# Kernel optimization log

Hardware: AMD Instinct MI355X
Metric: run time of the kernel (lower is better)

The kernel has to match this reference:

```python
import jax, jax.numpy as jnp
import numpy as np

N = 20000
N_RET = 20000
NEG_SLOPE = 0.2


def _xavier(key, shape):
    fan_in, fan_out = shape[-2], shape[-1]
    limit = float(np.sqrt(6.0 / (fan_in + fan_out)))
    return jax.random.uniform(key, shape, jnp.float32, -limit, limit)


def setup_inputs() -> dict:
    key = jax.random.key(0)
    ks = jax.random.split(key, 24)
    E = 320000
    inp = {
        "emb_u": jax.random.normal(ks[0], (N, 256), jnp.float32),
        "emb_t": jax.random.normal(ks[1], (N, 256), jnp.float32),
        "src_u": jax.random.randint(ks[2], (E,), 0, N, jnp.int32),
        "trg_u": jax.random.randint(ks[3], (E,), 0, N, jnp.int32),
        "src_t": jax.random.randint(ks[4], (E,), 0, N, jnp.int32),
        "trg_t": jax.random.randint(ks[5], (E,), 0, N, jnp.int32),
    }
    # SpGATLayer params per stack (u=user graph, t=tweet graph), 2 layers each.
    # layer0: f_in=256, layer1: f_in = 64*4 = 256 (concat of heads); f_out=64, H=4.
    i = 6
    for side in ("u", "t"):
        for l in range(2):
            inp[f"w_{side}{l}"] = _xavier(ks[i], (4, 256, 64)); i += 1
            inp[f"a_src_{side}{l}"] = _xavier(ks[i], (4, 64, 1))[:, :, 0]; i += 1
            inp[f"a_trg_{side}{l}"] = _xavier(ks[i], (4, 64, 1))[:, :, 0]; i += 1
    inp["fc_w"] = _xavier(ks[i], (128, 16)); i += 1  # [in_features, out_features]
    inp["fc_b"] = jnp.zeros((16,), jnp.float32)
    return inp


def gat_layer(h, w, a_src, a_trg, src, trg):
    # h: [n, f_in], w: [H, f_in, F], a_*: [H, F]
    hp = jnp.einsum("nf,hfo->hno", h, w)                 # [H, n, F]
    attn_src = jnp.einsum("hno,ho->nh", hp, a_src)        # [n, H]
    attn_trg = jnp.einsum("hno,ho->nh", hp, a_trg)        # [n, H]
    e = jax.nn.leaky_relu(attn_src[src] + attn_trg[trg], NEG_SLOPE)  # [E, H]
    exp_e = jnp.exp(e - jnp.max(e))
    denom = jax.ops.segment_sum(exp_e, trg, num_segments=N)[trg] + 1e-16
    attn = (exp_e / denom)[:, :, None]                    # [E, H, 1]
    hp_lift = jnp.transpose(hp, (1, 0, 2))[src]           # [E, H, F]
    return jax.ops.segment_sum(hp_lift * attn, trg, num_segments=N)  # [n, H, F]


def run_stack(h, src, trg, w0, as0, at0, w1, as1, at1):
    x = gat_layer(h, w0, as0, at0, src, trg)
    x = jax.nn.elu(x.reshape(N, -1))                      # [n, H*F]
    x = gat_layer(x, w1, as1, at1, src, trg)
    return x.mean(axis=1)                                 # [n, F]


def reference(emb_u, emb_t, src_u, trg_u, src_t, trg_t,
              w_u0, a_src_u0, a_trg_u0, w_u1, a_src_u1, a_trg_u1,
              w_t0, a_src_t0, a_trg_t0, w_t1, a_src_t1, a_trg_t1,
              fc_w, fc_b):
    out_u = run_stack(emb_u, src_u, trg_u, w_u0, a_src_u0, a_trg_u0, w_u1, a_src_u1, a_trg_u1)
    out_t = run_stack(emb_t, src_t, trg_t, w_t0, a_src_t0, a_trg_t0, w_t1, a_src_t1, a_trg_t1)
    ret = jnp.concatenate([out_u[:N_RET], out_t[:N_RET]], axis=-1)   # [n_ret, 128]
    logits = ret @ fc_w + fc_b                                       # [n_ret, 16]
    return jax.nn.log_softmax(logits, axis=-1)
```

## Files before the change

### kernel.cpp

```cpp
#include <hip/hip_runtime.h>
#include <hip/hip_bf16.h>

#define NEG_SLOPE 0.2f

typedef unsigned short u16;
typedef u16 u16x8 __attribute__((ext_vector_type(8)));
typedef u16 u16x4 __attribute__((ext_vector_type(4)));
typedef short s16x8 __attribute__((ext_vector_type(8)));
typedef float f32x4 __attribute__((ext_vector_type(4)));

__device__ __forceinline__ u16 f2bf(float x) {
    unsigned u = __float_as_uint(x);
    return (u16)((u + 0x7fffu + ((u >> 16) & 1u)) >> 16);
}
__device__ __forceinline__ float bf2f(u16 h) {
    return __uint_as_float(((unsigned)h) << 16);
}

__global__ __launch_bounds__(256) void splitx_k(
    const float* __restrict__ x0, const float* __restrict__ x1,
    u16* __restrict__ Xh, u16* __restrict__ Xl, int per_side4)
{
    int i = blockIdx.x * 256 + threadIdx.x;
    if (i >= per_side4) return;
    int side = blockIdx.y;
    const float* X = side ? x1 : x0;
    size_t o = (size_t)side * per_side4 * 4 + (size_t)i * 4;
    float4 v = *(const float4*)(X + (size_t)i * 4);
    float f[4] = { v.x, v.y, v.z, v.w };
    u16x4 hi, lo;
    #pragma unroll
    for (int j = 0; j < 4; ++j) {
        u16 h = f2bf(f[j]);
        hi[j] = h;
        lo[j] = f2bf(f[j] - bf2f(h));
    }
    *(u16x4*)(Xh + o) = hi;
    *(u16x4*)(Xl + o) = lo;
}

__global__ __launch_bounds__(256) void wsplit4_k(
    const float* __restrict__ w0, const float* __restrict__ w1,
    const float* __restrict__ w2, const float* __restrict__ w3,
    u16* __restrict__ Wht, u16* __restrict__ Wlt)
{
    int tid = blockIdx.x * 256 + threadIdx.x;
    int which = tid >> 16;
    int idx = tid & 65535;
    const float* W = (which == 0) ? w0 : (which == 1) ? w1 : (which == 2) ? w2 : w3;
    int f = idx & 63, k = (idx >> 6) & 255, h = idx >> 14;
    float x = W[idx];
    u16 hi = f2bf(x);
    u16 lo = f2bf(x - bf2f(hi));
    int o = (which << 16) + (h * 64 + f) * 256 + k;
    Wht[o] = hi; Wlt[o] = lo;
}

__global__ __launch_bounds__(256) void gemm_mfma_k(
    const u16* __restrict__ xh_all, const u16* __restrict__ xl_all,
    const u16* __restrict__ Wht, const u16* __restrict__ Wlt,
    const float* __restrict__ au_s, const float* __restrict__ au_t,
    const float* __restrict__ at_s, const float* __restrict__ at_t,
    u16* __restrict__ hpb_all,
    float* __restrict__ asat,
    int layer, int n)
{
    const int side = blockIdx.y;
    const int row0 = blockIdx.x * 64;
    const int t = threadIdx.x;
    const int l = t & 63;
    const int h = t >> 6;
    const int which = side * 2 + layer;

    const u16* Xh = xh_all + (size_t)side * n * 256;
    const u16* Xl = xl_all + (size_t)side * n * 256;
    const u16* Wh = Wht + ((size_t)which << 16);
    const u16* Wl = Wlt + ((size_t)which << 16);
    const float* a_src = (side ? at_s : au_s) + h * 64;
    const float* a_trg = (side ? at_t : au_t) + h * 64;
    u16* HPB = hpb_all + (size_t)side * n * 256;
    float* as_ = asat + (size_t)which * n * 8;
    float* at_ = as_ + (size_t)n * 4;

    __shared__ u16 Ah[64 * 40], Al[64 * 40], Bh[256 * 40], Bl[256 * 40];

    const int sr = t >> 2, sp = t & 3;
    const int arow = (row0 + sr < n) ? (row0 + sr) : (n - 1);
    const u16* gAh = Xh + (size_t)arow * 256 + sp * 8;
    const u16* gAl = Xl + (size_t)arow * 256 + sp * 8;
    const int lda = sr * 40 + sp * 8;

    const int fb = l & 15;
    const int kg = l >> 4;
    int ra[4], cb[4];
    #pragma unroll
    for (int r = 0; r < 4; ++r) ra[r] = (r * 16 + fb) * 40 + kg * 8;
    #pragma unroll
    for (int c = 0; c < 4; ++c) cb[c] = (h * 64 + c * 16 + fb) * 40 + kg * 8;

    f32x4 acc[4][4];
    #pragma unroll
    for (int r = 0; r < 4; ++r)
        #pragma unroll
        for (int c = 0; c < 4; ++c) acc[r][c] = f32x4{0.f, 0.f, 0.f, 0.f};

    for (int k0 = 0; k0 < 256; k0 += 32) {
        __syncthreads();
        *(u16x8*)&Ah[lda] = *(const u16x8*)(gAh + k0);
        *(u16x8*)&Al[lda] = *(const u16x8*)(gAl + k0);
        #pragma unroll
        for (int i = 0; i < 4; ++i) {
            int j = t + i * 256;
            int col = j >> 2, cp = j & 3;
            int ofs = col * 40 + cp * 8;
            *(u16x8*)&Bh[ofs] = *(const u16x8*)(Wh + (size_t)col * 256 + k0 + cp * 8);
            *(u16x8*)&Bl[ofs] = *(const u16x8*)(Wl + (size_t)col * 256 + k0 + cp * 8);
        }
        __syncthreads();

        s16x8 bh[4], bl[4];
        #pragma unroll
        for (int c = 0; c < 4; ++c) {
            bh[c] = *(const s16x8*)&Bh[cb[c]];
            bl[c] = *(const s16x8*)&Bl[cb[c]];
        }
        #pragma unroll
        for (int r = 0; r < 4; ++r) {
            s16x8 ah = *(const s16x8*)&Ah[ra[r]];
            s16x8 al = *(const s16x8*)&Al[ra[r]];
            #pragma unroll
            for (int c = 0; c < 4; ++c) {
                acc[r][c] = __builtin_amdgcn_mfma_f32_16x16x32_bf16(ah, bh[c], acc[r][c], 0, 0, 0);
                acc[r][c] = __builtin_amdgcn_mfma_f32_16x16x32_bf16(ah, bl[c], acc[r][c], 0, 0, 0);
                acc[r][c] = __builtin_amdgcn_mfma_f32_16x16x32_bf16(al, bh[c], acc[r][c], 0, 0, 0);
            }
        }
    }

    float pav[4], pbv[4];
    #pragma unroll
    for (int c = 0; c < 4; ++c) { pav[c] = a_src[c * 16 + fb]; pbv[c] = a_trg[c * 16 + fb]; }

    #pragma unroll
    for (int r = 0; r < 4; ++r) {
        #pragma unroll
        for (int q = 0; q < 4; ++q) {
            int grow = row0 + r * 16 + kg * 4 + q;
            float s = 0.f, u = 0.f;
            if (grow < n) {
                u16* hrow = HPB + (size_t)grow * 256 + h * 64 + fb;
                #pragma unroll
                for (int c = 0; c < 4; ++c) {
                    float v = acc[r][c][q];
                    s += v * pav[c];
                    u += v * pbv[c];
                    hrow[c * 16] = f2bf(v);
                }
            }
            #pragma unroll
            for (int off = 8; off; off >>= 1) {
                s += __shfl_xor(s, off, 16);
                u += __shfl_xor(u, off, 16);
            }
            if (grow < n && fb == 0) {
                as_[grow * 4 + h] = s;
                at_[grow * 4 + h] = u;
            }
        }
    }
}

__global__ void hist2_k(const int* __restrict__ tu, const int* __restrict__ tt,
                        int* __restrict__ counts, int* __restrict__ ranks,
                        int E, int N)
{
    int e = blockIdx.x * blockDim.x + threadIdx.x;
    if (e < E)          ranks[e] = atomicAdd(&counts[tu[e]], 1);
    else if (e < 2 * E) ranks[e] = atomicAdd(&counts[N + tt[e - E]], 1);
}

__global__ __launch_bounds__(1024) void scan2_k(const int* __restrict__ counts_all,
                                                int* __restrict__ starts_all, int n)
{
    const int T = 1024;
    const int* counts = counts_all + blockIdx.x * n;
    int* starts = starts_all + blockIdx.x * (n + 1);
    int t = threadIdx.x;
    int chunk = (n + T - 1) / T;
    int beg = t * chunk;
    int end = min(beg + chunk, n);
    int sum = 0;
    for (int i = beg; i < end; ++i) sum += counts[i];
    __shared__ int lds[T];
    lds[t] = sum;
    __syncthreads();
    for (int off = 1; off < T; off <<= 1) {
        int v = (t >= off) ? lds[t - off] : 0;
        __syncthreads();
        lds[t] += v;
        __syncthreads();
    }
    int run = lds[t] - sum;
    for (int i = beg; i < end; ++i) { starts[i] = run; run += counts[i]; }
    if (t == T - 1) starts[n] = lds[T - 1];
}

__global__ void scatter2_k(const int* __restrict__ su, const int* __restrict__ st,
                           const int* __restrict__ tu, const int* __restrict__ tt,
                           const int* __restrict__ starts_all,
                           const int* __restrict__ ranks, int* __restrict__ srcs,
                           int E, int N)
{
    int e = blockIdx.x * blockDim.x + threadIdx.x;
    if (e < E) {
        srcs[starts_all[tu[e]] + ranks[e]] = su[e];
    } else if (e < 2 * E) {
        int ee = e - E;
        const int* st1 = starts_all + (N + 1);
        srcs[E + st1[tt[ee]] + ranks[e]] = st[ee];
    }
}

template<int LAYER>
__global__ __launch_bounds__(256) void aggregate_k(
    const u16* __restrict__ hpb_all, const float* __restrict__ asat,
    const int* __restrict__ starts2, const int* __restrict__ srcs2,
    u16* __restrict__ oh_all, u16* __restrict__ ol_all,
    float* __restrict__ of_all, int n, int E)
{
    const int side = blockIdx.y;
    const int w = threadIdx.x >> 6;
    const int l = threadIdx.x & 63;
    const int v = blockIdx.x * 4 + w;
    if (v >= n) return;
    const int h = l >> 4;
    const int which = side * 2 + LAYER;

    const u16* HPB = hpb_all + (size_t)side * n * 256;
    const float* as_ = asat + (size_t)which * n * 8;
    const float* at_ = as_ + (size_t)n * 4;
    const int* starts = starts2 + side * (n + 1);
    const int* srcs = srcs2 + (size_t)side * E;

    const int s0 = starts[v], s1 = starts[v + 1];
    const float atv = at_[v * 4 + h];
    const size_t lo4 = (size_t)l * 4;

    float4 ac0 = make_float4(0.f, 0.f, 0.f, 0.f), ac1 = ac0, ac2 = ac0, ac3 = ac0;
    float dn0 = 0.f, dn1 = 0.f, dn2 = 0.f, dn3 = 0.f;

    for (int base = s0; base < s1; base += 64) {
        int m = min(64, s1 - base);
        int s_l = (base + l < s1) ? srcs[base + l] : 0;
        int i = 0;
        for (; i + 3 < m; i += 4) {
            int sa = __shfl(s_l, i, 64);
            int sb = __shfl(s_l, i + 1, 64);
            int sc = __shfl(s_l, i + 2, 64);
            int sd = __shfl(s_l, i + 3, 64);
            u16x4 va = *(const u16x4*)(HPB + (size_t)sa * 256 + lo4);
            u16x4 vb = *(const u16x4*)(HPB + (size_t)sb * 256 + lo4);
            u16x4 vc = *(const u16x4*)(HPB + (size_t)sc * 256 + lo4);
            u16x4 vd = *(const u16x4*)(HPB + (size_t)sd * 256 + lo4);
            float ea = as_[sa * 4 + h] + atv;
            float eb = as_[sb * 4 + h] + atv;
            float ec = as_[sc * 4 + h] + atv;
            float ed = as_[sd * 4 + h] + atv;
            ea = (ea > 0.f) ? ea : NEG_SLOPE * ea;
            eb = (eb > 0.f) ? eb : NEG_SLOPE * eb;
            ec = (ec > 0.f) ? ec : NEG_SLOPE * ec;
            ed = (ed > 0.f) ? ed : NEG_SLOPE * ed;
            float pA = expf(ea), pB = expf(eb), pC = expf(ec), pD = expf(ed);
            dn0 += pA; dn1 += pB; dn2 += pC; dn3 += pD;
            ac0.x += pA * bf2f(va[0]); ac0.y += pA * bf2f(va[1]);
            ac0.z += pA * bf2f(va[2]); ac0.w += pA * bf2f(va[3]);
            ac1.x += pB * bf2f(vb[0]); ac1.y += pB * bf2f(vb[1]);
            ac1.z += pB * bf2f(vb[2]); ac1.w += pB * bf2f(vb[3]);
            ac2.x += pC * bf2f(vc[0]); ac2.y += pC * bf2f(vc[1]);
            ac2.z += pC * bf2f(vc[2]); ac2.w += pC * bf2f(vc[3]);
            ac3.x += pD * bf2f(vd[0]); ac3.y += pD * bf2f(vd[1]);
            ac3.z += pD * bf2f(vd[2]); ac3.w += pD * bf2f(vd[3]);
        }
        for (; i < m; ++i) {
            int sa = __shfl(s_l, i, 64);
            u16x4 va = *(const u16x4*)(HPB + (size_t)sa * 256 + lo4);
            float ea = as_[sa * 4 + h] + atv;
            ea = (ea > 0.f) ? ea : NEG_SLOPE * ea;
            float pA = expf(ea);
            dn0 += pA;
            ac0.x += pA * bf2f(va[0]); ac0.y += pA * bf2f(va[1]);
            ac0.z += pA * bf2f(va[2]); ac0.w += pA * bf2f(va[3]);
        }
    }

    float4 acc = make_float4(ac0.x + ac1.x + ac2.x + ac3.x,
                             ac0.y + ac1.y + ac2.y + ac3.y,
                             ac0.z + ac1.z + ac2.z + ac3.z,
                             ac0.w + ac1.w + ac2.w + ac3.w);
    float r = 1.f / (dn0 + dn1 + dn2 + dn3 + 1e-16f);
    acc.x *= r; acc.y *= r; acc.z *= r; acc.w *= r;

    if (LAYER == 0) {
        u16* oh = oh_all + (size_t)side * n * 256;
        u16* ol = ol_all + (size_t)side * n * 256;
        float f[4] = { acc.x, acc.y, acc.z, acc.w };
        u16x4 hi, lo;
        #pragma unroll
        for (int c = 0; c < 4; ++c) {
            float e = (f[c] > 0.f) ? f[c] : expm1f(f[c]);
            u16 hh = f2bf(e);
            hi[c] = hh;
            lo[c] = f2bf(e - bf2f(hh));
        }
        *(u16x4*)(oh + (size_t)v * 256 + lo4) = hi;
        *(u16x4*)(ol + (size_t)v * 256 + lo4) = lo;
    } else {
        float* of = of_all + (size_t)side * n * 64;
        acc.x += __shfl_xor(acc.x, 16, 64); acc.y += __shfl_xor(acc.y, 16, 64);
        acc.z += __shfl_xor(acc.z, 16, 64); acc.w += __shfl_xor(acc.w, 16, 64);
        acc.x += __shfl_xor(acc.x, 32, 64); acc.y += __shfl_xor(acc.y, 32, 64);
        acc.z += __shfl_xor(acc.z, 32, 64); acc.w += __shfl_xor(acc.w, 32, 64);
        if (l < 16) {
            acc.x *= 0.25f; acc.y *= 0.25f; acc.z *= 0.25f; acc.w *= 0.25f;
            *(float4*)(of + (size_t)v * 64 + l * 4) = acc;
        }
    }
}

__global__ __launch_bounds__(256) void final_k(
    const float* __restrict__ out_u, const float* __restrict__ out_t,
    const float* __restrict__ fcw, const float* __restrict__ fcb,
    float* __restrict__ out, int nret)
{
    int gid = blockIdx.x * blockDim.x + threadIdx.x;
    int nn = gid >> 4;
    int j  = gid & 15;
    if (nn >= nret) return;
    const float* ru = out_u + (size_t)nn * 64;
    const float* rt = out_t + (size_t)nn * 64;
    float acc = fcb[j];
    #pragma unroll 8
    for (int k = 0; k < 64; ++k) acc += ru[k] * fcw[k * 16 + j];
    #pragma unroll 8
    for (int k = 0; k < 64; ++k) acc += rt[k] * fcw[(64 + k) * 16 + j];

    float m = acc;
    for (int off = 8; off; off >>= 1) m = fmaxf(m, __shfl_xor(m, off, 16));
    float ex = expf(acc - m);
    float s = ex;
    for (int off = 8; off; off >>= 1) s += __shfl_xor(s, off, 16);
    out[(size_t)nn * 16 + j] = acc - m - logf(s);
}

extern "C" void kernel_launch(void* const* d_in, const int* in_sizes, int n_in,
                              void* d_out, int out_size, void* d_ws, size_t ws_size,
                              hipStream_t stream)
{
    const int N = in_sizes[0] / 256;
    const int E = in_sizes[2];
    const int NRET = out_size / 16;

    const float* emb[2]  = { (const float*)d_in[0], (const float*)d_in[1] };
    const int*   srcI[2] = { (const int*)d_in[2], (const int*)d_in[4] };
    const int*   trgI[2] = { (const int*)d_in[3], (const int*)d_in[5] };
    const float* fcw = (const float*)d_in[18];
    const float* fcb = (const float*)d_in[19];

    char* p = (char*)d_ws;
    u16* hpb  = (u16*)p;    p += (size_t)2 * N * 256 * 2;
    u16* xh   = (u16*)p;    p += (size_t)2 * N * 256 * 2;
    u16* xl   = (u16*)p;    p += (size_t)2 * N * 256 * 2;
    u16* wht  = (u16*)p;    p += (size_t)4 * 65536 * 2;
    u16* wlt  = (u16*)p;    p += (size_t)4 * 65536 * 2;
    float* asat = (float*)p; p += (size_t)4 * N * 8 * 4;
    float* outs = (float*)p; p += (size_t)2 * N * 64 * 4;
    int* starts2 = (int*)p; p += (size_t)2 * (N + 1) * 4;
    int* counts2 = (int*)p; p += (size_t)2 * N * 4;
    int* ranks2  = (int*)p; p += (size_t)2 * E * 4;
    int* srcs2   = (int*)p; p += (size_t)2 * E * 4;

    const int E2B = (2 * E + 255) / 256;
    const dim3 gemm_grid((N + 63) / 64, 2);
    const dim3 split_grid((N * 64 + 255) / 256, 2);
    const dim3 agg_grid((N + 3) / 4, 2);

    hipMemsetAsync(counts2, 0, (size_t)2 * N * 4, stream);

    hist2_k<<<E2B, 256, 0, stream>>>(trgI[0], trgI[1], counts2, ranks2, E, N);
    scan2_k<<<2, 1024, 0, stream>>>(counts2, starts2, N);
    scatter2_k<<<E2B, 256, 0, stream>>>(srcI[0], srcI[1], trgI[0], trgI[1],
                                        starts2, ranks2, srcs2, E, N);

    wsplit4_k<<<1024, 256, 0, stream>>>(
        (const float*)d_in[6], (const float*)d_in[9],
        (const float*)d_in[12], (const float*)d_in[15], wht, wlt);

    splitx_k<<<split_grid, 256, 0, stream>>>(emb[0], emb[1], xh, xl, N * 64);

    for (int layer = 0; layer < 2; ++layer) {
        const float* au_s = (const float*)d_in[6 + 0 * 6 + layer * 3 + 1];
        const float* au_t = (const float*)d_in[6 + 0 * 6 + layer * 3 + 2];
        const float* at_s = (const float*)d_in[6 + 1 * 6 + layer * 3 + 1];
        const float* at_t = (const float*)d_in[6 + 1 * 6 + layer * 3 + 2];

        gemm_mfma_k<<<gemm_grid, 256, 0, stream>>>(
            xh, xl, wht, wlt, au_s, au_t, at_s, at_t, hpb, asat, layer, N);

        if (layer == 0)
            aggregate_k<0><<<agg_grid, 256, 0, stream>>>(
                hpb, asat, starts2, srcs2, xh, xl, nullptr, N, E);
        else
            aggregate_k<1><<<agg_grid, 256, 0, stream>>>(
                hpb, asat, starts2, srcs2, nullptr, nullptr, outs, N, E);
    }

    final_k<<<(NRET * 16 + 255) / 256, 256, 0, stream>>>(
        outs, outs + (size_t)N * 64, fcw, fcb, (float*)d_out, NRET);
}
```

Measured before the change: 384.4 us.

## Precompute per-edge attention exponentials in separate kernel before aggregation

Adds a pexp_k kernel that computes the leaky-relu and exp attention weight once per edge and head, storing them in a new edge-ordered p4 buffer. The scatter kernel now also writes target ids in CSR order so this kernel can run. The aggregate kernel then reads the precomputed weights and source indices directly instead of recomputing exp redundantly across 16 lanes per head, and it drops the shuffle-based index broadcast. In exchange there is an extra kernel launch per layer plus extra global traffic for p4 and trgs, and it switches from expf to __expf.

```diff
diff --git a/kernel.cpp b/kernel.cpp
--- a/kernel.cpp
+++ b/kernel.cpp
@@ -208,22 +208,50 @@
 __global__ void scatter2_k(const int* __restrict__ su, const int* __restrict__ st,
                            const int* __restrict__ tu, const int* __restrict__ tt,
                            const int* __restrict__ starts_all,
-                           const int* __restrict__ ranks, int* __restrict__ srcs,
+                           const int* __restrict__ ranks,
+                           int* __restrict__ srcs, int* __restrict__ trgs,
                            int E, int N)
 {
     int e = blockIdx.x * blockDim.x + threadIdx.x;
     if (e < E) {
-        srcs[starts_all[tu[e]] + ranks[e]] = su[e];
+        int pos = starts_all[tu[e]] + ranks[e];
+        srcs[pos] = su[e];
+        trgs[pos] = tu[e];
     } else if (e < 2 * E) {
         int ee = e - E;
         const int* st1 = starts_all + (N + 1);
-        srcs[E + st1[tt[ee]] + ranks[e]] = st[ee];
-    }
+        int pos = E + st1[tt[ee]] + ranks[e];
+        srcs[pos] = st[ee];
+        trgs[pos] = tt[ee];
+    }
+}
+
+__global__ __launch_bounds__(256) void pexp_k(
+    const int* __restrict__ srcs2, const int* __restrict__ trgs2,
+    const float* __restrict__ asat, float* __restrict__ p4,
+    int layer, int n, int E)
+{
+    int j = blockIdx.x * 256 + threadIdx.x;
+    if (j >= E) return;
+    int side = blockIdx.y;
+    const float* as_ = asat + (size_t)(side * 2 + layer) * n * 8;
+    const float* at_ = as_ + (size_t)n * 4;
+    int s = srcs2[(size_t)side * E + j];
+    int v = trgs2[(size_t)side * E + j];
+    float4 a = *(const float4*)(as_ + s * 4);
+    float4 b = *(const float4*)(at_ + v * 4);
+    float4 p;
+    float x;
+    x = a.x + b.x; p.x = __expf(fmaxf(x, NEG_SLOPE * x));
+    x = a.y + b.y; p.y = __expf(fmaxf(x, NEG_SLOPE * x));
+    x = a.z + b.z; p.z = __expf(fmaxf(x, NEG_SLOPE * x));
+    x = a.w + b.w; p.w = __expf(fmaxf(x, NEG_SLOPE * x));
+    *(float4*)(p4 + ((size_t)side * E + j) * 4) = p;
 }
 
 template<int LAYER>
 __global__ __launch_bounds__(256) void aggregate_k(
-    const u16* __restrict__ hpb_all, const float* __restrict__ asat,
+    const u16* __restrict__ hpb_all, const float* __restrict__ p4,
     const int* __restrict__ starts2, const int* __restrict__ srcs2,
     u16* __restrict__ oh_all, u16* __restrict__ ol_all,
     float* __restrict__ of_all, int n, int E)
@@ -234,63 +262,43 @@
     const int v = blockIdx.x * 4 + w;
     if (v >= n) return;
     const int h = l >> 4;
-    const int which = side * 2 + LAYER;
-
-    const u16* HPB = hpb_all + (size_t)side * n * 256;
-    const float* as_ = asat + (size_t)which * n * 8;
-    const float* at_ = as_ + (size_t)n * 4;
+
+    const u16* hp_l = hpb_all + (size_t)side * n * 256 + l * 4;
     const int* starts = starts2 + side * (n + 1);
     const int* srcs = srcs2 + (size_t)side * E;
+    const float* pp = p4 + (size_t)side * E * 4 + h;
 
     const int s0 = starts[v], s1 = starts[v + 1];
-    const float atv = at_[v * 4 + h];
-    const size_t lo4 = (size_t)l * 4;
 
     float4 ac0 = make_float4(0.f, 0.f, 0.f, 0.f), ac1 = ac0, ac2 = ac0, ac3 = ac0;
     float dn0 = 0.f, dn1 = 0.f, dn2 = 0.f, dn3 = 0.f;
 
-    for (int base = s0; base < s1; base += 64) {
-        int m = min(64, s1 - base);
-        int s_l = (base + l < s1) ? srcs[base + l] : 0;
-        int i = 0;
-        for (; i + 3 < m; i += 4) {
-            int sa = __shfl(s_l, i, 64);
-            int sb = __shfl(s_l, i + 1, 64);
-            int sc = __shfl(s_l, i + 2, 64);
-            int sd = __shfl(s_l, i + 3, 64);
-            u16x4 va = *(const u16x4*)(HPB + (size_t)sa * 256 + lo4);
-            u16x4 vb = *(const u16x4*)(HPB + (size_t)sb * 256 + lo4);
-            u16x4 vc = *(const u16x4*)(HPB + (size_t)sc * 256 + lo4);
-            u16x4 vd = *(const u16x4*)(HPB + (size_t)sd * 256 + lo4);
-            float ea = as_[sa * 4 + h] + atv;
-            float eb = as_[sb * 4 + h] + atv;
-            float ec = as_[sc * 4 + h] + atv;
-            float ed = as_[sd * 4 + h] + atv;
-            ea = (ea > 0.f) ? ea : NEG_SLOPE * ea;
-            eb = (eb > 0.f) ? eb : NEG_SLOPE * eb;
-            ec = (ec > 0.f) ? ec : NEG_SLOPE * ec;
-            ed = (ed > 0.f) ? ed : NEG_SLOPE * ed;
-            float pA = expf(ea), pB = expf(eb), pC = expf(ec), pD = expf(ed);
-            dn0 += pA; dn1 += pB; dn2 += pC; dn3 += pD;
-            ac0.x += pA * bf2f(va[0]); ac0.y += pA * bf2f(va[1]);
-            ac0.z += pA * bf2f(va[2]); ac0.w += pA * bf2f(va[3]);
-            ac1.x += pB * bf2f(vb[0]); ac1.y += pB * bf2f(vb[1]);
-            ac1.z += pB * bf2f(vb[2]); ac1.w += pB * bf2f(vb[3]);
-            ac2.x += pC * bf2f(vc[0]); ac2.y += pC * bf2f(vc[1]);
-            ac2.z += pC * bf2f(vc[2]); ac2.w += pC * bf2f(vc[3]);
-            ac3.x += pD * bf2f(vd[0]); ac3.y += pD * bf2f(vd[1]);
-            ac3.z += pD * bf2f(vd[2]); ac3.w += pD * bf2f(vd[3]);
-        }
-        for (; i < m; ++i) {
-            int sa = __shfl(s_l, i, 64);
-            u16x4 va = *(const u16x4*)(HPB + (size_t)sa * 256 + lo4);
-            float ea = as_[sa * 4 + h] + atv;
-            ea = (ea > 0.f) ? ea : NEG_SLOPE * ea;
-            float pA = expf(ea);
-            dn0 += pA;
-            ac0.x += pA * bf2f(va[0]); ac0.y += pA * bf2f(va[1]);
-            ac0.z += pA * bf2f(va[2]); ac0.w += pA * bf2f(va[3]);
-        }
+    int j = s0;
+    for (; j + 3 < s1; j += 4) {
+        int sa = srcs[j], sb = srcs[j + 1], sc = srcs[j + 2], sd = srcs[j + 3];
+        float pA = pp[(j + 0) * 4], pB = pp[(j + 1) * 4];
+        float pC = pp[(j + 2) * 4], pD = pp[(j + 3) * 4];
+        u16x4 va = *(const u16x4*)(hp_l + sa * 256);
+        u16x4 vb = *(const u16x4*)(hp_l + sb * 256);
+        u16x4 vc = *(const u16x4*)(hp_l + sc * 256);
+        u16x4 vd = *(const u16x4*)(hp_l + sd * 256);
+        dn0 += pA; dn1 += pB; dn2 += pC; dn3 += pD;
+        ac0.x += pA * bf2f(va[0]); ac0.y += pA * bf2f(va[1]);
+        ac0.z += pA * bf2f(va[2]); ac0.w += pA * bf2f(va[3]);
+        ac1.x += pB * bf2f(vb[0]); ac1.y += pB * bf2f(vb[1]);
+        ac1.z += pB * bf2f(vb[2]); ac1.w += pB * bf2f(vb[3]);
+        ac2.x += pC * bf2f(vc[0]); ac2.y += pC * bf2f(vc[1]);
+        ac2.z += pC * bf2f(vc[2]); ac2.w += pC * bf2f(vc[3]);
+        ac3.x += pD * bf2f(vd[0]); ac3.y += pD * bf2f(vd[1]);
+        ac3.z += pD * bf2f(vd[2]); ac3.w += pD * bf2f(vd[3]);
+    }
+    for (; j < s1; ++j) {
+        int sa = srcs[j];
+        float pA = pp[j * 4];
+        u16x4 va = *(const u16x4*)(hp_l + sa * 256);
+        dn0 += pA;
+        ac0.x += pA * bf2f(va[0]); ac0.y += pA * bf2f(va[1]);
+        ac0.z += pA * bf2f(va[2]); ac0.w += pA * bf2f(va[3]);
     }
 
     float4 acc = make_float4(ac0.x + ac1.x + ac2.x + ac3.x,
@@ -312,8 +320,8 @@
             hi[c] = hh;
             lo[c] = f2bf(e - bf2f(hh));
         }
-        *(u16x4*)(oh + (size_t)v * 256 + lo4) = hi;
-        *(u16x4*)(ol + (size_t)v * 256 + lo4) = lo;
+        *(u16x4*)(oh + (size_t)v * 256 + l * 4) = hi;
+        *(u16x4*)(ol + (size_t)v * 256 + l * 4) = lo;
     } else {
         float* of = of_all + (size_t)side * n * 64;
         acc.x += __shfl_xor(acc.x, 16, 64); acc.y += __shfl_xor(acc.y, 16, 64);
@@ -374,22 +382,25 @@
     u16* wlt  = (u16*)p;    p += (size_t)4 * 65536 * 2;
     float* asat = (float*)p; p += (size_t)4 * N * 8 * 4;
     float* outs = (float*)p; p += (size_t)2 * N * 64 * 4;
+    float* p4   = (float*)p; p += (size_t)2 * E * 4 * 4;
     int* starts2 = (int*)p; p += (size_t)2 * (N + 1) * 4;
     int* counts2 = (int*)p; p += (size_t)2 * N * 4;
     int* ranks2  = (int*)p; p += (size_t)2 * E * 4;
     int* srcs2   = (int*)p; p += (size_t)2 * E * 4;
+    int* trgs2   = (int*)p; p += (size_t)2 * E * 4;
 
     const int E2B = (2 * E + 255) / 256;
     const dim3 gemm_grid((N + 63) / 64, 2);
     const dim3 split_grid((N * 64 + 255) / 256, 2);
     const dim3 agg_grid((N + 3) / 4, 2);
+    const dim3 pexp_grid((E + 255) / 256, 2);
 
     hipMemsetAsync(counts2, 0, (size_t)2 * N * 4, stream);
 
     hist2_k<<<E2B, 256, 0, stream>>>(trgI[0], trgI[1], counts2, ranks2, E, N);
     scan2_k<<<2, 1024, 0, stream>>>(counts2, starts2, N);
     scatter2_k<<<E2B, 256, 0, stream>>>(srcI[0], srcI[1], trgI[0], trgI[1],
-                                        starts2, ranks2, srcs2, E, N);
+                                        starts2, ranks2, srcs2, trgs2, E, N);
 
     wsplit4_k<<<1024, 256, 0, stream>>>(
         (const float*)d_in[6], (const float*)d_in[9],
@@ -406,12 +417,14 @@
         gemm_mfma_k<<<gemm_grid, 256, 0, stream>>>(
             xh, xl, wht, wlt, au_s, au_t, at_s, at_t, hpb, asat, layer, N);
 
+        pexp_k<<<pexp_grid, 256, 0, stream>>>(srcs2, trgs2, asat, p4, layer, N, E);
+
         if (layer == 0)
             aggregate_k<0><<<agg_grid, 256, 0, stream>>>(
-                hpb, asat, starts2, srcs2, xh, xl, nullptr, N, E);
+                hpb, p4, starts2, srcs2, xh, xl, nullptr, N, E);
         else
             aggregate_k<1><<<agg_grid, 256, 0, stream>>>(
-                hpb, asat, starts2, srcs2, nullptr, nullptr, outs, N, E);
+                hpb, p4, starts2, srcs2, nullptr, nullptr, outs, N, E);
     }
 
     final_k<<<(NRET * 16 + 255) / 256, 256, 0, stream>>>(
```

Result: no change. 384.9 us (+0.1%).
